# Kernel tuning notes

Hardware: AMD Instinct MI355X
Metric: run time of the kernel (lower is better)

## Reference

```python
import jax, jax.numpy as jnp
import numpy as np

EPS = 1e-5

def bn(x, p, axis):
    # p: (4,C) = [gamma, beta, running_mean, running_var]; eval-mode batchnorm
    g, b, m, v = p
    shp = [1] * x.ndim
    shp[axis] = -1
    g = g.reshape(shp); b = b.reshape(shp); m = m.reshape(shp); v = v.reshape(shp)
    return (x - m) * g * jax.lax.rsqrt(v + EPS) + b

def knn_idx(query, ref, k):
    # query (B,S,D), ref (B,N,D) -> (B,S,k) nearest-neighbor indices
    d = (jnp.sum(query * query, -1)[:, :, None]
         - 2.0 * jnp.einsum('bsd,bnd->bsn', query, ref)
         + jnp.sum(ref * ref, -1)[:, None, :])
    return jax.lax.top_k(-d, k)[1]

def fps(xyz, npoint):
    # farthest point sampling, deterministic start at index 0. xyz (B,N,3) -> (B,npoint)
    B, N, _ = xyz.shape
    def body(i, state):
        idxs, dists, far = state
        idxs = idxs.at[:, i].set(far)
        centroid = jnp.take_along_axis(xyz, far[:, None, None], axis=1)  # (B,1,3)
        d = jnp.sum((xyz - centroid) ** 2, -1)                           # (B,N)
        dists = jnp.minimum(dists, d)
        return idxs, dists, jnp.argmax(dists, -1).astype(jnp.int32)
    idxs = jnp.zeros((B, npoint), jnp.int32)
    dists = jnp.full((B, N), 1e10, xyz.dtype)
    far = jnp.zeros((B,), jnp.int32)
    idxs, _, _ = jax.lax.fori_loop(0, npoint, body, (idxs, dists, far))
    return idxs

def sample_and_group(npoint, nsample, xyz, feature):
    # xyz (B,N,3); feature (B,C,N) channel-first -> new_xyz (B,S,3), new_feature (B,S,k,2C)
    B = xyz.shape[0]
    xyz_sg = jax.lax.stop_gradient(xyz)
    fps_idx = fps(xyz_sg, npoint)                       # (B,S)
    bi = jnp.arange(B)[:, None]
    new_xyz = xyz[bi, fps_idx]                          # (B,S,3)
    ft = jnp.swapaxes(feature, 1, 2)                    # (B,N,C)
    new_pts = ft[bi, fps_idx]                           # (B,S,C)
    idx = knn_idx(jax.lax.stop_gradient(new_xyz), xyz_sg, nsample)  # (B,S,k)
    grouped = ft[jnp.arange(B)[:, None, None], idx]     # (B,S,k,C)
    centered = grouped - new_pts[:, :, None, :]
    new_feature = jnp.concatenate(
        [centered, jnp.broadcast_to(new_pts[:, :, None, :], grouped.shape)], -1)
    return new_xyz, new_feature

def local_op(x, w, bnp):
    # x (B,S,k,D); conv1d k=1 over D, bn, relu, max over neighbors -> (B,out,S)
    h = jax.nn.relu(bn(jnp.einsum('bskd,od->bsko', x, w), bnp, -1))
    return jnp.swapaxes(jnp.max(h, axis=2), 1, 2)

def edge_branch(f_t, idx, w, bnp):
    # DGCNN-style EdgeConv: concat(f_j - f_i, f_i), conv2d k=1, bn, leakyrelu, max over k
    B = f_t.shape[0]
    nb = f_t[jnp.arange(B)[:, None, None], idx]         # (B,N,k,C)
    center = jnp.broadcast_to(f_t[:, :, None, :], nb.shape)
    e = jnp.concatenate([nb - center, center], -1)      # (B,N,k,2C)
    h = jax.nn.leaky_relu(bn(jnp.einsum('bnkc,oc->bnko', e, w), bnp, -1), 0.2)
    return jnp.max(h, axis=2)                           # (B,N,C)

def dual_graph_fusion(xyz_cf, f, k, geo_w, geo_bn, feat_w, feat_bn, fuse_w, fuse_bn):
    # xyz_cf (B,3,N), f (B,C,N): one kNN graph in coordinate space, one in feature space,
    # EdgeConv on each, concat, 1x1 conv fusion -> (B,C,N)
    xyz_t = jax.lax.stop_gradient(jnp.swapaxes(xyz_cf, 1, 2))  # (B,N,3)
    f_t = jnp.swapaxes(f, 1, 2)                                # (B,N,C)
    idx_g = knn_idx(xyz_t, xyz_t, k)
    f_sg = jax.lax.stop_gradient(f_t)
    idx_f = knn_idx(f_sg, f_sg, k)
    g = edge_branch(f_t, idx_g, geo_w, geo_bn)
    h = edge_branch(f_t, idx_f, feat_w, feat_bn)
    fused = jnp.concatenate([g, h], -1)                        # (B,N,2C)
    out = jax.nn.leaky_relu(bn(jnp.einsum('bnc,oc->bno', fused, fuse_w), fuse_bn, -1), 0.2)
    return jnp.swapaxes(out, 1, 2)                             # (B,C,N)

def _bn_params(key, c):
    k1, k2, k3, k4 = jax.random.split(key, 4)
    g = jax.random.uniform(k1, (c,), minval=0.5, maxval=1.5)
    b = jax.random.normal(k2, (c,)) * 0.1
    m = jax.random.normal(k3, (c,)) * 0.1
    v = jax.random.uniform(k4, (c,), minval=0.5, maxval=1.5)
    return jnp.stack([g, b, m, v])

def setup_inputs() -> dict:
    key = jax.random.key(0)
    ks = jax.random.split(key, 20)
    B, N = 16, 2048
    def w(k, o, i):
        return jax.random.normal(k, (o, i), dtype=jnp.float32) * (1.0 / np.sqrt(i))
    return {
        'x': jax.random.normal(ks[0], (B, 6, N), dtype=jnp.float32),
        'w1': w(ks[1], 64, 6),        'bn1': _bn_params(ks[2], 64),
        'w2': w(ks[3], 1024, 64),     'bn2': _bn_params(ks[4], 1024),
        'geo_w': w(ks[5], 64, 128),   'geo_bn': _bn_params(ks[6], 64),
        'feat_w': w(ks[7], 64, 128),  'feat_bn': _bn_params(ks[8], 64),
        'fuse_w': w(ks[9], 64, 128),  'fuse_bn': _bn_params(ks[10], 64),
        'gl0_w': w(ks[11], 128, 128), 'gl0_bn': _bn_params(ks[12], 128),
        'gl1_w': w(ks[13], 256, 256), 'gl1_bn': _bn_params(ks[14], 256),
        'wf': w(ks[15], 512, 1280),   'bnf': _bn_params(ks[16], 512),
    }

def reference(x, w1, bn1, w2, bn2, geo_w, geo_bn, feat_w, feat_bn, fuse_w, fuse_bn,
              gl0_w, gl0_bn, gl1_w, gl1_bn, wf, bnf):
    B, _, N = x.shape
    xyz = jnp.swapaxes(x[:, 0:3, :], 1, 2)                                   # (B,N,3)
    f_o = jax.nn.relu(bn(jnp.einsum('bcn,oc->bon', x, w1), bn1, 1))          # (B,64,N)
    out_feat = dual_graph_fusion(x[:, 0:3, :], f_o, 20,
                                 geo_w, geo_bn, feat_w, feat_bn, fuse_w, fuse_bn)
    stride = N // 256
    x_skip = jax.nn.relu(bn(jnp.einsum('bcn,oc->bon', f_o[:, :, ::stride], w2), bn2, 1))  # (B,1024,256)
    new_xyz, nf = sample_and_group(512, 32, xyz, out_feat)
    f0 = local_op(nf, gl0_w, gl0_bn)                                         # (B,128,512)
    new_xyz, nf = sample_and_group(256, 32, new_xyz, f0)
    f1 = local_op(nf, gl1_w, gl1_bn)                                         # (B,256,256)
    f1 = jnp.concatenate([f1, x_skip], 1)                                    # (B,1280,256)
    res = jax.nn.leaky_relu(bn(jnp.einsum('bcn,oc->bon', f1, wf), bnf, 1), 0.2)  # (B,512,256)
    return res
```

## Files before the change

kernel.cpp:

```cpp
#include <hip/hip_runtime.h>
#include <float.h>
#include <math.h>


static constexpr int B_   = 16;
static constexpr int N_   = 2048;
static constexpr int NP1  = 512;
static constexpr int NP2  = 256;
static constexpr int KG   = 20;
static constexpr int NSAMP= 32;
static constexpr int CHQ  = 256;

static constexpr long OFF_FT   = 0;
static constexpr long OFF_SQ   = OFF_FT   + (long)B_*N_*64;
static constexpr long OFF_BIG  = OFF_SQ   + (long)B_*N_;
static constexpr long OFF_IDXG = OFF_BIG  + (long)B_*N_*256;
static constexpr long OFF_IDXF = OFF_IDXG + (long)B_*N_*KG;
static constexpr long OFF_OUTF = OFF_IDXF + (long)B_*N_*KG;
static constexpr long OFF_FPS1 = OFF_OUTF + (long)B_*N_*64;
static constexpr long OFF_NX1  = OFF_FPS1 + (long)B_*NP1;
static constexpr long OFF_IDX1 = OFF_NX1  + (long)B_*NP1*3;
static constexpr long OFF_F0T  = OFF_IDX1 + (long)B_*NP1*NSAMP;
static constexpr long OFF_FPS2 = OFF_F0T  + (long)B_*NP1*128;
static constexpr long OFF_NX2  = OFF_FPS2 + (long)B_*NP2;
static constexpr long OFF_IDX2 = OFF_NX2  + (long)B_*NP2*3;
static constexpr long OFF_Q1   = OFF_IDX2 + (long)B_*NP2*NSAMP;
static constexpr long OFF_V    = OFF_Q1   + (long)B_*NP1*512;
static constexpr long OFF_WPP  = OFF_V    + (long)B_*NP2*1280;
static constexpr long OFF_WPQ0 = OFF_WPP  + 256*64;
static constexpr long OFF_WPQ1 = OFF_WPQ0 + 256*64;
static constexpr long OFF_WFT  = OFF_WPQ1 + 512*128;
static constexpr long OFF_SC   = OFF_WFT  + 128*64;
static constexpr long OFF_DL1  = OFF_SC   + 4352;
static constexpr long OFF_DL2  = OFF_DL1  + (long)B_*256*8;
static constexpr long OFF_ST   = OFF_DL2  + (long)B_*512;
static constexpr long OFF_GSQ  = OFF_ST   + 256;

static constexpr int SC_S1=0, SC_T1=64, SC_SGEO=128, SC_TGEO=192, SC_SFEAT=256, SC_TFEAT=320,
   SC_SFUSE=384, SC_TFUSE=448, SC_SGL0=512, SC_TGL0=640, SC_SGL1=768, SC_TGL1=1024,
   SC_S2=1280, SC_T2=2304, SC_SF=3328, SC_TF=3840;

__device__ __forceinline__ float lrelu_(float x) { return x >= 0.0f ? x : 0.2f * x; }

template<int CTRL, int RM>
__device__ __forceinline__ float dpp_maxm(float v) {
    int o = __builtin_amdgcn_update_dpp(__float_as_int(v), __float_as_int(v),
                                        CTRL, RM, 0xF, false);
    return fmaxf(v, __int_as_float(o));
}
__device__ __forceinline__ float wave_max64_sgpr(float v) {
    v = dpp_maxm<0xB1, 0xF>(v);
    v = dpp_maxm<0x4E, 0xF>(v);
    v = dpp_maxm<0x141,0xF>(v);
    v = dpp_maxm<0x140,0xF>(v);
    v = dpp_maxm<0x142,0xA>(v);
    v = dpp_maxm<0x143,0xC>(v);
    return __int_as_float(__builtin_amdgcn_readlane(__float_as_int(v), 63));
}

template<int CTRL>
__device__ __forceinline__ unsigned dpp_minu(unsigned x) {
    unsigned o = (unsigned)__builtin_amdgcn_update_dpp(0, (int)x, CTRL, 0xF, 0xF, true);
    return o < x ? o : x;
}
__device__ __forceinline__ unsigned wave_minu(unsigned x) {
    x = dpp_minu<0xB1>(x);
    x = dpp_minu<0x4E>(x);
    x = dpp_minu<0x141>(x);
    x = dpp_minu<0x140>(x);
    { unsigned o = (unsigned)__shfl_xor((int)x, 16); x = o < x ? o : x; }
    { unsigned o = (unsigned)__shfl_xor((int)x, 32); x = o < x ? o : x; }
    return x;
}

__device__ __forceinline__ unsigned sortable_(float f) {
    unsigned u = __float_as_uint(f);
    return u ^ ((unsigned)((int)u >> 31) | 0x80000000u);
}

__global__ void k_prep(const float* __restrict__ bn1, const float* __restrict__ bn2,
                       const float* __restrict__ geow, const float* __restrict__ geobn,
                       const float* __restrict__ featw, const float* __restrict__ featbn,
                       const float* __restrict__ fusew, const float* __restrict__ fusebn,
                       const float* __restrict__ gl0w, const float* __restrict__ gl0bn,
                       const float* __restrict__ gl1w, const float* __restrict__ gl1bn,
                       const float* __restrict__ bnfp, float* __restrict__ ws)
{
    const int tid = blockIdx.x * blockDim.x + threadIdx.x;
    const int nt  = gridDim.x * blockDim.x;
    float* sc = ws + OFF_SC;
    {
        const float* ps[8]  = {bn1, geobn, featbn, fusebn, gl0bn, gl1bn, bn2, bnfp};
        const int    ch[8]  = {64, 64, 64, 64, 128, 256, 1024, 512};
        const int    so[8]  = {SC_S1, SC_SGEO, SC_SFEAT, SC_SFUSE, SC_SGL0, SC_SGL1, SC_S2, SC_SF};
        const int    to[8]  = {SC_T1, SC_TGEO, SC_TFEAT, SC_TFUSE, SC_TGL0, SC_TGL1, SC_T2, SC_TF};
        for (int g = 0; g < 8; g++) {
            const float* p = ps[g]; int C = ch[g];
            for (int i = tid; i < C; i += nt) {
                float gg = p[i], bb = p[C+i], mm = p[2*C+i], vv = p[3*C+i];
                float s = gg * (1.0f / sqrtf(vv + 1e-5f));
                sc[so[g] + i] = s;
                sc[to[g] + i] = bb - mm * s;
            }
        }
    }
    for (int j = tid; j < 256*64; j += nt) {
        int o = j >> 6, c = j & 63; float v;
        if      (o < 64)  v = geow[o*128 + c];
        else if (o < 128) v = geow[(o-64)*128 + 64 + c];
        else if (o < 192) v = featw[(o-128)*128 + c];
        else              v = featw[(o-192)*128 + 64 + c];
        ws[OFF_WPP + j] = v;
    }
    for (int j = tid; j < 256*64; j += nt) {
        int o = j >> 6, c = j & 63; float v;
        if (o < 128) v = gl0w[o*128 + c];
        else         v = gl0w[(o-128)*128 + 64 + c] - gl0w[(o-128)*128 + c];
        ws[OFF_WPQ0 + j] = v;
    }
    for (int j = tid; j < 512*128; j += nt) {
        int o = j >> 7, c = j & 127; float v;
        if (o < 256) v = gl1w[o*256 + c];
        else         v = gl1w[(o-256)*256 + 128 + c] - gl1w[(o-256)*256 + c];
        ws[OFF_WPQ1 + j] = v;
    }
    for (int j = tid; j < 128*64; j += nt) {
        int c = j >> 6, o = j & 63;
        ws[OFF_WFT + j] = fusew[o*128 + c];
    }
}

__global__ void __launch_bounds__(256) k_feat0(const float* __restrict__ x,
                                               const float* __restrict__ w1,
                                               const float* __restrict__ sc,
                                               float* __restrict__ ft, float* __restrict__ sq,
                                               float* __restrict__ gsq)
{
    const int t = threadIdx.x, lane = t & 63, w = t >> 6;
    const int pid = blockIdx.x*4 + w;
    const int b = pid >> 11, n = pid & (N_-1);
    const float* xb = x + (long)b*6*N_ + n;
    float acc = 0.0f;
    #pragma unroll
    for (int c = 0; c < 6; c++) acc += w1[lane*6 + c] * xb[(long)c*N_];
    float val = fmaxf(sc[SC_S1 + lane]*acc + sc[SC_T1 + lane], 0.0f);
    ft[((long)b*N_ + n)*64 + lane] = val;
    float v2 = val*val;
    #pragma unroll
    for (int s = 1; s < 64; s <<= 1) v2 += __shfl_xor(v2, s);
    if (lane == 0) {
        sq[b*N_ + n] = v2;
        float rx = xb[0], ry = xb[N_], rz = xb[2*N_];
        gsq[b*N_ + n] = __fadd_rn(__fadd_rn(__fmul_rn(rx,rx), __fmul_rn(ry,ry)),
                                  __fmul_rn(rz,rz));
    }
}

template<int RPL, int KSEL>
__device__ __forceinline__ void topk_sel3(float (&v)[RPL], int lane, int* __restrict__ out)
{
    unsigned key[RPL];
    #pragma unroll
    for (int j = 0; j < RPL; j++) key[j] = sortable_(v[j]);

    unsigned consumed = 0;
    unsigned m1 = key[0]; int s1 = 0;
    unsigned m2 = 0xFFFFFFFFu; int s2 = 0;
    #pragma unroll
    for (int j = 1; j < RPL; j++) {
        unsigned kk = key[j];
        bool lt1 = kk < m1;
        bool lt2 = kk < m2;
        unsigned nm2 = lt1 ? m1 : (lt2 ? kk : m2);
        int      ns2 = lt1 ? s1 : (lt2 ? j  : s2);
        m1 = lt1 ? kk : m1;
        s1 = lt1 ? j  : s1;
        m2 = nm2; s2 = ns2;
    }
    #pragma unroll 1
    for (int k = 0; k < KSEL; k++) {
        unsigned g = wave_minu(m1);
        unsigned long long cand = __ballot(m1 == g);
        int gi;
        if (__popcll(cand) > 1) {
            int ci = (m1 == g) ? (s1*64 + lane) : 0x7FFFFFFF;
            #pragma unroll
            for (int s = 1; s < 64; s <<= 1) { int o = __shfl_xor(ci, s); ci = o < ci ? o : ci; }
            gi = ci;
        } else {
            int wl = __ffsll((long long)cand) - 1;
            gi = __builtin_amdgcn_readlane(s1, wl) * 64 + wl;
        }
        if (lane == 0) out[k] = gi;
        if (k + 1 < KSEL) {
            bool win = (m1 == g) && (s1*64 + lane == gi);
            if (win) {
                consumed |= 1u << s1;
                m1 = m2; s1 = s2;
                m2 = 0xFFFFFFFFu;
            }
            bool need = win && (m1 == 0xFFFFFFFFu);
            if (__any(need)) {
                if (need) {
                    m1 = 0xFFFFFFFFu; s1 = 0; m2 = 0xFFFFFFFFu; s2 = 0;
                    #pragma unroll
                    for (int j = 0; j < RPL; j++) {
                        unsigned kk = ((consumed >> j) & 1u) ? 0xFFFFFFFFu : key[j];
                        bool lt1 = kk < m1;
                        bool lt2 = kk < m2;
                        unsigned nm2 = lt1 ? m1 : (lt2 ? kk : m2);
                        int      ns2 = lt1 ? s1 : (lt2 ? j  : s2);
                        m1 = lt1 ? kk : m1;
                        s1 = lt1 ? j  : s1;
                        m2 = nm2; s2 = ns2;
                    }
                }
            }
        }
    }
}

template<int NREF, int RPL, int KSEL, bool RSQ>
__device__ __forceinline__ void knn_gbody(
    const float* qp, long qBatch, int qsN, int qsD, int NQ,
    const float* rp, long rBatch, long rsN, long rsD,
    const float* rsq, long rsqBatch,
    int* out, int bid)
{
    const int t = threadIdx.x, lane = t & 63, w = t >> 6;
    const int bpb = NQ / 4;
    const int b = bid / bpb;
    const int qi = (bid % bpb)*4 + w;
    const float* rb = rp + (long)b*rBatch;
    const float* qb = qp + (long)b*qBatch + (long)qi*qsN;
    float qx = qb[0], qy = qb[qsD], qz = qb[2*qsD];
    float sumq = __fadd_rn(__fadd_rn(__fmul_rn(qx,qx), __fmul_rn(qy,qy)), __fmul_rn(qz,qz));
    float v[RPL];
    #pragma unroll
    for (int j = 0; j < RPL; j++) {
        long n = j*64 + lane;
        float rx = rb[n*rsN];
        float ry = rb[n*rsN + rsD];
        float rz = rb[n*rsN + 2*rsD];
        float dot = __fadd_rn(__fadd_rn(__fmul_rn(qx,rx), __fmul_rn(qy,ry)), __fmul_rn(qz,rz));
        float sumr;
        if constexpr (RSQ) sumr = rsq[(long)b*rsqBatch + n];
        else sumr = __fadd_rn(__fadd_rn(__fmul_rn(rx,rx), __fmul_rn(ry,ry)), __fmul_rn(rz,rz));
        v[j] = __fadd_rn(__fsub_rn(sumq, __fmul_rn(2.0f, dot)), sumr);
    }
    topk_sel3<RPL, KSEL>(v, lane, out + ((long)b*NQ + qi)*KSEL);
}

__device__ __forceinline__ void fps1_seg_body(
    const float* __restrict__ x, int b, int i0, int cnt,
    int* __restrict__ fps1, float* __restrict__ nx1,
    float* __restrict__ dl1s, float* __restrict__ st, float* __restrict__ smem)
{
    __builtin_amdgcn_s_setprio(3);
    const int t = threadIdx.x, lane = t & 63, wave = t >> 6;
    const float* pb = x + (long)b*6*N_;

    float4* mrgc   = (float4*)smem;
    int*    mrgi   = (int*)(smem + 32);
    int*    sidxsg = (int*)(smem + 40);
    float*  mxsg   = smem + 296;
    float*  mysg   = smem + 552;
    float*  mzsg   = smem + 808;

    float px[8], py[8], pz[8], dl[8];
    {
        const float4* a4  = (const float4*)(pb + 8*t);
        const float4* b4  = (const float4*)(pb + N_ + 8*t);
        const float4* c4p = (const float4*)(pb + 2*N_ + 8*t);
        float4 a0 = a4[0], a1 = a4[1];
        float4 b0 = b4[0], b1 = b4[1];
        float4 c0 = c4p[0], c1 = c4p[1];
        px[0]=a0.x; px[1]=a0.y; px[2]=a0.z; px[3]=a0.w;
        px[4]=a1.x; px[5]=a1.y; px[6]=a1.z; px[7]=a1.w;
        py[0]=b0.x; py[1]=b0.y; py[2]=b0.z; py[3]=b0.w;
        py[4]=b1.x; py[5]=b1.y; py[6]=b1.z; py[7]=b1.w;
        pz[0]=c0.x; pz[1]=c0.y; pz[2]=c0.z; pz[3]=c0.w;
        pz[4]=c1.x; pz[5]=c1.y; pz[6]=c1.z; pz[7]=c1.w;
    }
    int far; float cx, cy, cz;
    if (i0 == 0) {
        #pragma unroll
        for (int p = 0; p < 8; p++) dl[p] = 1e10f;
        far = 0; cx = pb[0]; cy = pb[N_]; cz = pb[2*N_];
    } else {
        const float4* ds = (const float4*)(dl1s + ((long)b*256 + t)*8);
        float4 d0 = ds[0], d1 = ds[1];
        dl[0]=d0.x; dl[1]=d0.y; dl[2]=d0.z; dl[3]=d0.w;
        dl[4]=d1.x; dl[5]=d1.y; dl[6]=d1.z; dl[7]=d1.w;
        far = __float_as_int(st[b*16+0]);
        cx = st[b*16+1]; cy = st[b*16+2]; cz = st[b*16+3];
    }

    for (int k = 0; k < cnt; k++) {
        if (t == 0) { sidxsg[k] = far; mxsg[k] = cx; mysg[k] = cy; mzsg[k] = cz; }
        float bv = -1.0f; int bp = 0;
        #pragma unroll
        for (int p = 0; p < 8; p++) {
            float dx = __fsub_rn(px[p], cx);
            float dy = __fsub_rn(py[p], cy);
            float dz = __fsub_rn(pz[p], cz);
            float d  = __fadd_rn(__fadd_rn(__fmul_rn(dx,dx), __fmul_rn(dy,dy)), __fmul_rn(dz,dz));
            float nd = fminf(dl[p], d);
            dl[p] = nd;
            if (nd > bv) { bv = nd; bp = p; }
        }
        float wx = px[0], wy = py[0], wz = pz[0];
        #pragma unroll
        for (int p = 1; p < 8; p++) {
            bool c = (bp == p);
            wx = c ? px[p] : wx; wy = c ? py[p] : wy; wz = c ? pz[p] : wz;
        }
        float gm = wave_max64_sgpr(bv);
        unsigned long long cand = __ballot(bv == gm);
        int wl = __ffsll((long long)cand) - 1;
        int   wbp = __builtin_amdgcn_readlane(bp, wl);
        float sxw = __int_as_float(__builtin_amdgcn_readlane(__float_as_int(wx), wl));
        float syw = __int_as_float(__builtin_amdgcn_readlane(__float_as_int(wy), wl));
        float szw = __int_as_float(__builtin_amdgcn_readlane(__float_as_int(wz), wl));
        int par = k & 1;
        if (lane == 0) {
            mrgc[par*4 + wave] = make_float4(sxw, syw, szw, gm);
            mrgi[par*4 + wave] = (((wave << 6) | wl) << 3) + wbp;
        }
        __syncthreads();
        float4 e0 = mrgc[par*4 + 0];
        float fv = e0.w; int fi = mrgi[par*4 + 0];
        float ncx = e0.x, ncy = e0.y, ncz = e0.z;
        #pragma unroll
// ... 153 lines not shown
        acc[1][0] += a.y*b4.x; acc[1][1] += a.y*b4.y; acc[1][2] += a.y*b4.z; acc[1][3] += a.y*b4.w;
        acc[2][0] += a.z*b4.x; acc[2][1] += a.z*b4.y; acc[2][2] += a.z*b4.z; acc[2][3] += a.z*b4.w;
        acc[3][0] += a.w*b4.x; acc[3][1] += a.w*b4.y; acc[3][2] += a.w*b4.z; acc[3][3] += a.w*b4.w;
    }
    const int i0 = ib*64 + ty*4;
    const int j0 = jb*64 + tx*4;
    #pragma unroll
    for (int ii = 0; ii < 4; ii++) {
        float sqq = sqb[qbNew + i0 + ii];
        #pragma unroll
        for (int jj = 0; jj < 4; jj++) {
            int r = j0 + jj;
            Dnew[((long)b*CHQ + i0 + ii)*N_ + r] = (sqq - 2.0f*acc[ii][jj]) + sqb[r];
        }
    }
}

__device__ __forceinline__ void proj64_body(
    int gi, int nIB, int nJB,
    const float* __restrict__ A, long aBatch, int aRow,
    const float* __restrict__ Bw,
    float* __restrict__ C, long cBatch, int cRow, int cCol0,
    int act, const float* __restrict__ sv, const float* __restrict__ tv,
    float* __restrict__ smem)
{
    float* As = smem;
    float* Bs = smem + 4096;
    const int ib = gi % nIB;
    const int jb = (gi / nIB) % nJB;
    const int b  = gi / (nIB*nJB);
    const int t  = threadIdx.x;
    const int tx = t & 15, ty = t >> 4;
    const float* Ab = A + (long)b*aBatch + (long)(ib*64)*aRow;
    #pragma unroll
    for (int m = 0; m < 4; m++) {
        int li = t + m*256; int r = li >> 4; int c4 = li & 15;
        int cs = r ^ ((c4 & 7) << 2);
        float4 av = *(const float4*)(Ab + (long)r*aRow + c4*4);
        As[(c4*4+0)*64 + cs] = av.x; As[(c4*4+1)*64 + cs] = av.y;
        As[(c4*4+2)*64 + cs] = av.z; As[(c4*4+3)*64 + cs] = av.w;
        float4 bv = *(const float4*)(Bw + (long)(jb*64 + r)*64 + c4*4);
        Bs[(c4*4+0)*64 + cs] = bv.x; Bs[(c4*4+1)*64 + cs] = bv.y;
        Bs[(c4*4+2)*64 + cs] = bv.z; Bs[(c4*4+3)*64 + cs] = bv.w;
    }
    __syncthreads();
    float acc[4][4];
    #pragma unroll
    for (int i = 0; i < 4; i++)
        #pragma unroll
        for (int j = 0; j < 4; j++) acc[i][j] = 0.0f;
    #pragma unroll 4
    for (int k = 0; k < 64; k++) {
        int s4 = ((k >> 2) & 7) << 2;
        float4 a  = *(const float4*)&As[k*64 + ((ty*4) ^ s4)];
        float4 b4 = *(const float4*)&Bs[k*64 + ((tx*4) ^ s4)];
        acc[0][0] += a.x*b4.x; acc[0][1] += a.x*b4.y; acc[0][2] += a.x*b4.z; acc[0][3] += a.x*b4.w;
        acc[1][0] += a.y*b4.x; acc[1][1] += a.y*b4.y; acc[1][2] += a.y*b4.z; acc[1][3] += a.y*b4.w;
        acc[2][0] += a.z*b4.x; acc[2][1] += a.z*b4.y; acc[2][2] += a.z*b4.z; acc[2][3] += a.z*b4.w;
        acc[3][0] += a.w*b4.x; acc[3][1] += a.w*b4.y; acc[3][2] += a.w*b4.z; acc[3][3] += a.w*b4.w;
    }
    const int i0 = ib*64 + ty*4;
    const int j0 = jb*64 + tx*4;
    #pragma unroll
    for (int ii = 0; ii < 4; ii++)
        #pragma unroll
        for (int jj = 0; jj < 4; jj++) {
            int j = j0 + jj;
            float vv = acc[ii][jj];
            if (act == 1) vv = fmaxf(sv[j]*vv + tv[j], 0.0f);
            C[(long)b*cBatch + (long)(i0+ii)*cRow + cCol0 + j] = vv;
        }
}

__device__ __forceinline__ void sel_body(
    const float* __restrict__ Dold, int qbOld, int* __restrict__ idxf, int bid)
{
    const int t = threadIdx.x, lane = t & 63, w = t >> 6;
    const int r = bid*4 + w;
    const int b = r >> 8, qi = r & (CHQ-1);
    const float* row = Dold + ((long)b*CHQ + qi) * N_;
    float v[32];
    #pragma unroll
    for (int j = 0; j < 32; j++) v[j] = row[j*64 + lane];
    topk_sel3<32, KG>(v, lane, idxf + ((long)b*N_ + qbOld + qi)*KG);
}

__device__ __forceinline__ void edgefuse_body(
    const float* __restrict__ P, const int* __restrict__ idxg, const int* __restrict__ idxf,
    const float* __restrict__ wft, const float* __restrict__ sc,
    float* __restrict__ outf, int bid, float* __restrict__ smem)
{
    float* wt = smem;
    float* fused = smem + 8192;
    const int t = threadIdx.x, lane = t & 63, w = t >> 6;
    for (int i = t; i < 128*64; i += 256) wt[i] = wft[i];
    const int pid = bid*4 + w;
    const int b = pid >> 11, n = pid & (N_-1);
    const float* Prow = P + ((long)b*N_ + n)*256;
    const int* ig  = idxg + ((long)b*N_ + n)*KG;
    const int* ifx = idxf + ((long)b*N_ + n)*KG;
    float gmax = -FLT_MAX, hmax = -FLT_MAX;
    for (int k = 0; k < KG; k++) {
        int idg = ig[k];
        gmax = fmaxf(gmax, P[((long)b*N_ + idg)*256 + lane]);
        int idf = ifx[k];
        hmax = fmaxf(hmax, P[((long)b*N_ + idf)*256 + 128 + lane]);
    }
    float glin = gmax - Prow[lane]       + Prow[64 + lane];
    float hlin = hmax - Prow[128 + lane] + Prow[192 + lane];
    float gv = lrelu_(sc[SC_SGEO + lane]*glin + sc[SC_TGEO + lane]);
    float hv = lrelu_(sc[SC_SFEAT + lane]*hlin + sc[SC_TFEAT + lane]);
    fused[w*128 + lane]      = gv;
    fused[w*128 + 64 + lane] = hv;
    __syncthreads();
    float acc = 0.0f;
    #pragma unroll 8
    for (int c4 = 0; c4 < 32; c4++) {
        float4 f = *(const float4*)&fused[w*128 + c4*4];
        acc += f.x * wt[(c4*4+0)*64 + lane];
        acc += f.y * wt[(c4*4+1)*64 + lane];
        acc += f.z * wt[(c4*4+2)*64 + lane];
        acc += f.w * wt[(c4*4+3)*64 + lane];
    }
    float ov = lrelu_(sc[SC_SFUSE + lane]*acc + sc[SC_TFUSE + lane]);
    outf[((long)b*N_ + n)*64 + lane] = ov;
}

template<int QN, int ROWW, int CO, int MROWS, int SO>
__device__ __forceinline__ void gathermax_body(
    const float* __restrict__ Q, const int* __restrict__ knn, const int* __restrict__ fpsi,
    const float* __restrict__ sv, const float* __restrict__ tv,
    float* __restrict__ outp, int outRow, int bid)
{
    const int t = threadIdx.x, lane = t & 63, w = t >> 6;
    const int pid = bid*4 + w;
    const int b = pid / SO, s = pid % SO;
    const int* ix = knn + ((long)b*SO + s)*NSAMP;
    float mx[QN];
    #pragma unroll
    for (int q = 0; q < QN; q++) mx[q] = -FLT_MAX;
    for (int k = 0; k < NSAMP; k++) {
        int id = ix[k];
        const float* r = Q + ((long)b*MROWS + id)*ROWW;
        #pragma unroll
        for (int q = 0; q < QN; q++) mx[q] = fmaxf(mx[q], r[lane + 64*q]);
    }
    int crow = fpsi[b*SO + s];
    const float* cr = Q + ((long)b*MROWS + crow)*ROWW + CO;
    #pragma unroll
    for (int q = 0; q < QN; q++) {
        int o = lane + 64*q;
        float lin = mx[q] + cr[o];
        float val = fmaxf(sv[o]*lin + tv[o], 0.0f);
        outp[((long)b*SO + s)*outRow + o] = val;
    }
}

__global__ void __launch_bounds__(256, 4) k_geo0(
    const float* __restrict__ x, int* __restrict__ idxg,
    int* __restrict__ fps1, float* __restrict__ nx1,
    float* __restrict__ dl1s, float* __restrict__ st,
    const float* __restrict__ ft, const float* __restrict__ sq,
    const float* __restrict__ gsq, float* __restrict__ D0)
{
    __shared__ float smem[8192];
    if (blockIdx.x < (unsigned)B_) {
        fps1_seg_body(x, blockIdx.x, 0, 256, fps1, nx1, dl1s, st, smem);
        return;
    }
    if (blockIdx.x < (unsigned)(B_ + 8192)) {
        knn_gbody<N_,32,KG,true>(x, (long)6*N_, 1, N_, N_,
                                 x, (long)6*N_, 1, N_,
                                 gsq, (long)N_, idxg, blockIdx.x - B_);
        return;
    }
    dist_gemm_body(ft, sq, D0, 0, blockIdx.x - (B_ + 8192), smem);
}

__global__ void __launch_bounds__(256, 4) k_chain(
    const float* __restrict__ x, const float* __restrict__ ft, const float* __restrict__ sq,
    float* __restrict__ Dnew, int qbNew,
    const float* __restrict__ Dold, int qbOld,
    int* __restrict__ idxf,
    int* __restrict__ fps1, float* __restrict__ nx1,
    float* __restrict__ dl1s, float* __restrict__ st, int i0)
{
    __shared__ float smem[8192];
    if (blockIdx.x < 16u) {
        fps1_seg_body(x, blockIdx.x, i0, 32, fps1, nx1, dl1s, st, smem);
        return;
    }
    if (blockIdx.x < 1040u) {
        sel_body(Dold, qbOld, idxf, blockIdx.x - 16);
        return;
    }
    dist_gemm_body(ft, sq, Dnew, qbNew, blockIdx.x - 1040, smem);
}

__global__ void __launch_bounds__(256, 4) k_tail9(
    const float* __restrict__ x, const float* __restrict__ ft,
    const float* __restrict__ Dold, int qbOld, int* __restrict__ idxf,
    int* __restrict__ fps1, float* __restrict__ nx1,
    float* __restrict__ dl1s, float* __restrict__ st,
    const float* __restrict__ wpp, float* __restrict__ big)
{
    __shared__ float smem[8192];
    if (blockIdx.x < 16u) {
        fps1_seg_body(x, blockIdx.x, 480, 32, fps1, nx1, dl1s, st, smem);
        return;
    }
    if (blockIdx.x < 1040u) {
        sel_body(Dold, qbOld, idxf, blockIdx.x - 16);
        return;
    }
    proj64_body(blockIdx.x - 1040, 32, 4, ft, (long)N_*64, 64, wpp,
                big, (long)N_*256, 256, 0, 0, nullptr, nullptr, smem);
}

__global__ void __launch_bounds__(256, 4) k_tail10(
    const float* __restrict__ nx1, int* __restrict__ fps2, float* __restrict__ nx2,
    float* __restrict__ dl2s, float* __restrict__ st,
    const float* __restrict__ P, const int* __restrict__ idxg, const int* __restrict__ idxf,
    const float* __restrict__ wft, const float* __restrict__ sc, float* __restrict__ outf,
    const float* __restrict__ ft, const float* __restrict__ w2, float* __restrict__ V)
{
    __shared__ float smem[8704];
    if (blockIdx.x < 16u) {
        fps2_seg_body(blockIdx.x, 0, 128, nx1, fps2, nx2, dl2s, st, smem);
        return;
    }
    if (blockIdx.x < (unsigned)(16 + 8192)) {
        edgefuse_body(P, idxg, idxf, wft, sc, outf, blockIdx.x - 16, smem);
        return;
    }
    proj64_body(blockIdx.x - (16 + 8192), 4, 16, ft, (long)N_*64, 512, w2,
                V, (long)NP2*1280, 1280, 256, 1, sc + SC_S2, sc + SC_T2, smem);
}

__global__ void __launch_bounds__(256, 4) k_tail11(
    const float* __restrict__ nx1, int* __restrict__ fps2, float* __restrict__ nx2,
    float* __restrict__ dl2s, float* __restrict__ st,
    const float* __restrict__ x, const float* __restrict__ gsq, int* __restrict__ idx1,
    const float* __restrict__ outf, const float* __restrict__ wpq0, float* __restrict__ big)
{
    __shared__ float smem[8192];
    if (blockIdx.x < 16u) {
        fps2_seg_body(blockIdx.x, 128, 128, nx1, fps2, nx2, dl2s, st, smem);
        return;
    }
    if (blockIdx.x < (unsigned)(16 + 2048)) {
        knn_gbody<2048,32,32,true>(nx1, (long)NP1*3, 3, 1, NP1,
                                   x, (long)6*N_, (long)1, (long)N_,
                                   gsq, (long)N_, idx1, blockIdx.x - 16);
        return;
    }
    proj64_body(blockIdx.x - (16 + 2048), 32, 4, outf, (long)N_*64, 64, wpq0,
                big, (long)N_*256, 256, 0, 0, nullptr, nullptr, smem);
}

__global__ void __launch_bounds__(256, 4) k_gm0knn2(
    const float* __restrict__ big, const int* __restrict__ idx1, const int* __restrict__ fps1,
    const float* __restrict__ sc, float* __restrict__ f0t,
    const float* __restrict__ nx2, const float* __restrict__ nx1, int* __restrict__ idx2)
{
    if (blockIdx.x < 2048u) {
        gathermax_body<2,256,128,2048,512>(big, idx1, fps1,
            sc + SC_SGL0, sc + SC_TGL0, f0t, 128, blockIdx.x);
        return;
    }
    knn_gbody<512,8,32,false>(nx2, (long)NP2*3, 3, 1, NP2,
                              nx1, (long)NP1*3, (long)3, (long)1,
                              nullptr, 0, idx2, blockIdx.x - 2048);
}

__global__ void __launch_bounds__(256) k_gemm(
    const float* __restrict__ A, long aBatch, int aRow,
    const float* __restrict__ Bw, long bBatch, int K,
    float* __restrict__ C, long cBatch, int cRow, int cCol0,
    int act, const float* __restrict__ sv, const float* __restrict__ tv,
    int epi)
{
    __shared__ float As[4096];
    __shared__ float Bs[4096];
    const int b  = blockIdx.z;
    const int ib = blockIdx.x * 64;
    const int jb = blockIdx.y * 64;
    const int t  = threadIdx.x;
    const int tx = t & 15, ty = t >> 4;
    const float* Ab = A + (long)b * aBatch;
    const float* Bb = Bw + (long)b * bBatch;
    float acc[4][4];
    #pragma unroll
    for (int i = 0; i < 4; i++)
        #pragma unroll
        for (int j = 0; j < 4; j++) acc[i][j] = 0.0f;

    for (int kb = 0; kb < K; kb += 64) {
        #pragma unroll
        for (int m = 0; m < 4; m++) {
            int li = t + m*256; int r = li >> 4; int c4 = li & 15;
            int cs = r ^ ((c4 & 7) << 2);
            float4 av = *(const float4*)(Ab + (long)(ib + r)*aRow + kb + c4*4);
            As[(c4*4+0)*64 + cs] = av.x; As[(c4*4+1)*64 + cs] = av.y;
            As[(c4*4+2)*64 + cs] = av.z; As[(c4*4+3)*64 + cs] = av.w;
            float4 bv = *(const float4*)(Bb + (long)(jb + r)*K + kb + c4*4);
            Bs[(c4*4+0)*64 + cs] = bv.x; Bs[(c4*4+1)*64 + cs] = bv.y;
            Bs[(c4*4+2)*64 + cs] = bv.z; Bs[(c4*4+3)*64 + cs] = bv.w;
        }
        __syncthreads();
        #pragma unroll 4
        for (int k = 0; k < 64; k++) {
            int s4 = ((k >> 2) & 7) << 2;
            float4 a  = *(const float4*)&As[k*64 + ((ty*4) ^ s4)];
            float4 b4 = *(const float4*)&Bs[k*64 + ((tx*4) ^ s4)];
            acc[0][0] += a.x*b4.x; acc[0][1] += a.x*b4.y; acc[0][2] += a.x*b4.z; acc[0][3] += a.x*b4.w;
            acc[1][0] += a.y*b4.x; acc[1][1] += a.y*b4.y; acc[1][2] += a.y*b4.z; acc[1][3] += a.y*b4.w;
            acc[2][0] += a.z*b4.x; acc[2][1] += a.z*b4.y; acc[2][2] += a.z*b4.z; acc[2][3] += a.z*b4.w;
            acc[3][0] += a.w*b4.x; acc[3][1] += a.w*b4.y; acc[3][2] += a.w*b4.z; acc[3][3] += a.w*b4.w;
        }
        __syncthreads();
    }

    const int i0 = ib + ty*4;
    const int j0 = jb + tx*4;
    if (epi == 2) {
        #pragma unroll
        for (int ii = 0; ii < 4; ii++)
            #pragma unroll
            for (int jj = 0; jj < 4; jj++) {
                int j = j0 + jj;
                float vv = lrelu_(sv[j]*acc[ii][jj] + tv[j]);
                C[(long)b*cBatch + (long)j*cRow + (i0+ii)] = vv;
            }
    } else {
        #pragma unroll
        for (int ii = 0; ii < 4; ii++)
            #pragma unroll
            for (int jj = 0; jj < 4; jj++) {
                int j = j0 + jj;
                float vv = acc[ii][jj];
                if (act == 1) vv = fmaxf(sv[j]*vv + tv[j], 0.0f);
                else if (act == 2) vv = lrelu_(sv[j]*vv + tv[j]);
                C[(long)b*cBatch + (long)(i0+ii)*cRow + cCol0 + j] = vv;
            }
    }
}

template<int QN, int ROWW, int CO, int MROWS, int SO>
__global__ void __launch_bounds__(256) k_gathermax(
    const float* __restrict__ Q, const int* __restrict__ knn, const int* __restrict__ fpsi,
    const float* __restrict__ sv, const float* __restrict__ tv,
    float* __restrict__ outp, int outRow)
{
    gathermax_body<QN,ROWW,CO,MROWS,SO>(Q, knn, fpsi, sv, tv, outp, outRow, blockIdx.x);
}

extern "C" void kernel_launch(void* const* d_in, const int* in_sizes, int n_in,
                              void* d_out, int out_size, void* d_ws, size_t ws_size,
                              hipStream_t stream)
{
    const float* x      = (const float*)d_in[0];
    const float* w1     = (const float*)d_in[1];
    const float* bn1    = (const float*)d_in[2];
    const float* w2     = (const float*)d_in[3];
    const float* bn2    = (const float*)d_in[4];
    const float* geow   = (const float*)d_in[5];
    const float* geobn  = (const float*)d_in[6];
    const float* featw  = (const float*)d_in[7];
    const float* featbn = (const float*)d_in[8];
    const float* fusew  = (const float*)d_in[9];
    const float* fusebn = (const float*)d_in[10];
    const float* gl0w   = (const float*)d_in[11];
    const float* gl0bn  = (const float*)d_in[12];
    const float* gl1w   = (const float*)d_in[13];
    const float* gl1bn  = (const float*)d_in[14];
    const float* wf     = (const float*)d_in[15];
    const float* bnfp   = (const float*)d_in[16];

    float* ws  = (float*)d_ws;
    float* out = (float*)d_out;

    float* FT   = ws + OFF_FT;
    float* SQ   = ws + OFF_SQ;
    float* BIG  = ws + OFF_BIG;
    int*   IDXG = (int*)(ws + OFF_IDXG);
    int*   IDXF = (int*)(ws + OFF_IDXF);
    float* OUTF = ws + OFF_OUTF;
    int*   FPS1 = (int*)(ws + OFF_FPS1);
    float* NX1  = ws + OFF_NX1;
    int*   IDX1 = (int*)(ws + OFF_IDX1);
    float* F0T  = ws + OFF_F0T;
    int*   FPS2 = (int*)(ws + OFF_FPS2);
    float* NX2  = ws + OFF_NX2;
    int*   IDX2 = (int*)(ws + OFF_IDX2);
    float* Q1B  = ws + OFF_Q1;
    float* V    = ws + OFF_V;
    float* WPP  = ws + OFF_WPP;
    float* WPQ0 = ws + OFF_WPQ0;
    float* WPQ1 = ws + OFF_WPQ1;
    float* WFT  = ws + OFF_WFT;
    float* SC   = ws + OFF_SC;
    float* DL1  = ws + OFF_DL1;
    float* DL2  = ws + OFF_DL2;
    float* ST   = ws + OFF_ST;
    float* GSQ  = ws + OFF_GSQ;

    hipLaunchKernelGGL(k_prep, dim3(64), dim3(256), 0, stream,
        bn1, bn2, geow, geobn, featw, featbn, fusew, fusebn, gl0w, gl0bn, gl1w, gl1bn, bnfp, ws);

    hipLaunchKernelGGL(k_feat0, dim3(B_*N_/4), dim3(256), 0, stream, x, w1, SC, FT, SQ, GSQ);

    hipLaunchKernelGGL(k_geo0, dim3(B_ + 8192 + 2048), dim3(256), 0, stream,
        x, IDXG, FPS1, NX1, DL1, ST, FT, SQ, GSQ, BIG);

    float* bufs[2] = { BIG, Q1B };
    for (int ci = 1; ci < 8; ci++) {
        hipLaunchKernelGGL(k_chain, dim3(16 + 1024 + 2048), dim3(256), 0, stream,
            x, FT, SQ,
            bufs[ci & 1], ci*CHQ,
            bufs[(ci - 1) & 1], (ci - 1)*CHQ,
            IDXF, FPS1, NX1, DL1, ST, 256 + 32*(ci - 1));
    }

    hipLaunchKernelGGL(k_tail9, dim3(16 + 1024 + 2048), dim3(256), 0, stream,
        x, FT, bufs[1], 7*CHQ, IDXF, FPS1, NX1, DL1, ST, WPP, BIG);

    hipLaunchKernelGGL(k_tail10, dim3(16 + 8192 + 1024), dim3(256), 0, stream,
        NX1, FPS2, NX2, DL2, ST,
        BIG, IDXG, IDXF, WFT, SC, OUTF,
        FT, w2, V);

    hipLaunchKernelGGL(k_tail11, dim3(16 + 2048 + 2048), dim3(256), 0, stream,
        NX1, FPS2, NX2, DL2, ST,
        x, GSQ, IDX1,
        OUTF, WPQ0, BIG);

    hipLaunchKernelGGL(k_gm0knn2, dim3(2048 + 1024), dim3(256), 0, stream,
        BIG, IDX1, FPS1, SC, F0T, NX2, NX1, IDX2);

    hipLaunchKernelGGL(k_gemm, dim3(NP1/64, 512/64, B_), dim3(256), 0, stream,
        F0T, (long)NP1*128, 128, WPQ1, (long)0, 128,
        Q1B, (long)NP1*512, 512, 0, 0, nullptr, nullptr, 0);

    hipLaunchKernelGGL((k_gathermax<4,512,256,512,256>), dim3(B_*NP2/4), dim3(256), 0, stream,
        Q1B, IDX2, FPS2, SC + SC_SGL1, SC + SC_TGL1, V, 1280);

    hipLaunchKernelGGL(k_gemm, dim3(NP2/64, 512/64, B_), dim3(256), 0, stream,
        V, (long)NP2*1280, 1280, wf, (long)0, 1280,
        out, (long)512*256, 256, 0, 2, SC + SC_SF, SC + SC_TF, 2);

    (void)in_sizes; (void)n_in; (void)out_size; (void)ws_size;
}
```

Measured before the change: 660.5 us.

## Pack xyz into float4, fuse prep/feat0 launch, deepen top-k candidate cache

Merges the prep and first-feature kernels into one launch. Point coordinates are now stored with their squared norm as a packed float4, so the kNN kernels do one vector load per reference point instead of four strided loads. The top-k selector now keeps three candidates per lane instead of two, which makes full rescans rarer. It also reduces the wave minimum with DPP row broadcasts and a readlane, and gathers results in registers for a single coalesced store. The cost is extra registers per lane and a little more work per compare step.

```diff
diff --git a/kernel.cpp b/kernel.cpp
--- a/kernel.cpp
+++ b/kernel.cpp
@@ -34,7 +34,7 @@
 static constexpr long OFF_DL1  = OFF_SC   + 4352;
 static constexpr long OFF_DL2  = OFF_DL1  + (long)B_*256*8;
 static constexpr long OFF_ST   = OFF_DL2  + (long)B_*512;
-static constexpr long OFF_GSQ  = OFF_ST   + 256;
+static constexpr long OFF_XYZ4 = OFF_ST   + 256;
 
 static constexpr int SC_S1=0, SC_T1=64, SC_SGEO=128, SC_TGEO=192, SC_SFEAT=256, SC_TFEAT=320,
    SC_SFUSE=384, SC_TFUSE=448, SC_SGL0=512, SC_TGL0=640, SC_SGL1=768, SC_TGL1=1024,
@@ -58,19 +58,19 @@
     return __int_as_float(__builtin_amdgcn_readlane(__float_as_int(v), 63));
 }
 
-template<int CTRL>
-__device__ __forceinline__ unsigned dpp_minu(unsigned x) {
-    unsigned o = (unsigned)__builtin_amdgcn_update_dpp(0, (int)x, CTRL, 0xF, 0xF, true);
+template<int CTRL, int RM>
+__device__ __forceinline__ unsigned dpp_minm(unsigned x) {
+    unsigned o = (unsigned)__builtin_amdgcn_update_dpp((int)x, (int)x, CTRL, RM, 0xF, false);
     return o < x ? o : x;
 }
-__device__ __forceinline__ unsigned wave_minu(unsigned x) {
-    x = dpp_minu<0xB1>(x);
-    x = dpp_minu<0x4E>(x);
-    x = dpp_minu<0x141>(x);
-    x = dpp_minu<0x140>(x);
-    { unsigned o = (unsigned)__shfl_xor((int)x, 16); x = o < x ? o : x; }
-    { unsigned o = (unsigned)__shfl_xor((int)x, 32); x = o < x ? o : x; }
-    return x;
+__device__ __forceinline__ unsigned wave_minu_sgpr(unsigned x) {
+    x = dpp_minm<0xB1, 0xF>(x);
+    x = dpp_minm<0x4E, 0xF>(x);
+    x = dpp_minm<0x141,0xF>(x);
+    x = dpp_minm<0x140,0xF>(x);
+    x = dpp_minm<0x142,0xA>(x);
+    x = dpp_minm<0x143,0xC>(x);
+    return (unsigned)__builtin_amdgcn_readlane((int)x, 63);
 }
 
 __device__ __forceinline__ unsigned sortable_(float f) {
@@ -78,16 +78,17 @@
     return u ^ ((unsigned)((int)u >> 31) | 0x80000000u);
 }
 
-__global__ void k_prep(const float* __restrict__ bn1, const float* __restrict__ bn2,
-                       const float* __restrict__ geow, const float* __restrict__ geobn,
-                       const float* __restrict__ featw, const float* __restrict__ featbn,
-                       const float* __restrict__ fusew, const float* __restrict__ fusebn,
-                       const float* __restrict__ gl0w, const float* __restrict__ gl0bn,
-                       const float* __restrict__ gl1w, const float* __restrict__ gl1bn,
-                       const float* __restrict__ bnfp, float* __restrict__ ws)
-{
-    const int tid = blockIdx.x * blockDim.x + threadIdx.x;
-    const int nt  = gridDim.x * blockDim.x;
+__device__ __forceinline__ void prep_body(
+    const float* bn1, const float* bn2,
+    const float* geow, const float* geobn,
+    const float* featw, const float* featbn,
+    const float* fusew, const float* fusebn,
+    const float* gl0w, const float* gl0bn,
+    const float* gl1w, const float* gl1bn,
+    const float* bnfp, float* ws, int bid)
+{
+    const int tid = bid * 256 + threadIdx.x;
+    const int nt  = 64 * 256;
     float* sc = ws + OFF_SC;
     {
         const float* ps[8]  = {bn1, geobn, featbn, fusebn, gl0bn, gl1bn, bn2, bnfp};
@@ -130,56 +131,81 @@
     }
 }
 
-__global__ void __launch_bounds__(256) k_feat0(const float* __restrict__ x,
-                                               const float* __restrict__ w1,
-                                               const float* __restrict__ sc,
-                                               float* __restrict__ ft, float* __restrict__ sq,
-                                               float* __restrict__ gsq)
+__device__ __forceinline__ void feat0_body(
+    const float* __restrict__ x, const float* __restrict__ w1,
+    const float* __restrict__ bn1,
+    float* __restrict__ ft, float* __restrict__ sq,
+    float4* __restrict__ xyz4, int bid)
 {
     const int t = threadIdx.x, lane = t & 63, w = t >> 6;
-    const int pid = blockIdx.x*4 + w;
+    const int pid = bid*4 + w;
     const int b = pid >> 11, n = pid & (N_-1);
     const float* xb = x + (long)b*6*N_ + n;
     float acc = 0.0f;
     #pragma unroll
     for (int c = 0; c < 6; c++) acc += w1[lane*6 + c] * xb[(long)c*N_];
-    float val = fmaxf(sc[SC_S1 + lane]*acc + sc[SC_T1 + lane], 0.0f);
+    float gg = bn1[lane], bb = bn1[64+lane], mm = bn1[128+lane], vv = bn1[192+lane];
+    float s = gg * (1.0f / sqrtf(vv + 1e-5f));
+    float tt = bb - mm * s;
+    float val = fmaxf(s*acc + tt, 0.0f);
     ft[((long)b*N_ + n)*64 + lane] = val;
     float v2 = val*val;
     #pragma unroll
-    for (int s = 1; s < 64; s <<= 1) v2 += __shfl_xor(v2, s);
+    for (int sft = 1; sft < 64; sft <<= 1) v2 += __shfl_xor(v2, sft);
     if (lane == 0) {
         sq[b*N_ + n] = v2;
         float rx = xb[0], ry = xb[N_], rz = xb[2*N_];
-        gsq[b*N_ + n] = __fadd_rn(__fadd_rn(__fmul_rn(rx,rx), __fmul_rn(ry,ry)),
-                                  __fmul_rn(rz,rz));
-    }
+        float g2 = __fadd_rn(__fadd_rn(__fmul_rn(rx,rx), __fmul_rn(ry,ry)), __fmul_rn(rz,rz));
+        xyz4[(long)b*N_ + n] = make_float4(rx, ry, rz, g2);
+    }
+}
+
+__global__ void __launch_bounds__(256) k_init(
+    const float* __restrict__ x, const float* __restrict__ w1,
+    const float* bn1, const float* bn2,
+    const float* geow, const float* geobn,
+    const float* featw, const float* featbn,
+    const float* fusew, const float* fusebn,
+    const float* gl0w, const float* gl0bn,
+    const float* gl1w, const float* gl1bn,
+    const float* bnfp, float* ws,
+    float* __restrict__ ft, float* __restrict__ sq, float4* __restrict__ xyz4)
+{
+    if (blockIdx.x < 64u) {
+        prep_body(bn1, bn2, geow, geobn, featw, featbn, fusew, fusebn,
+                  gl0w, gl0bn, gl1w, gl1bn, bnfp, ws, blockIdx.x);
+        return;
+    }
+    feat0_body(x, w1, bn1, ft, sq, xyz4, blockIdx.x - 64);
 }
 
 template<int RPL, int KSEL>
-__device__ __forceinline__ void topk_sel3(float (&v)[RPL], int lane, int* __restrict__ out)
+__device__ __forceinline__ void topk_sel4(float (&v)[RPL], int lane, int* __restrict__ out)
 {
     unsigned key[RPL];
     #pragma unroll
     for (int j = 0; j < RPL; j++) key[j] = sortable_(v[j]);
 
     unsigned consumed = 0;
-    unsigned m1 = key[0]; int s1 = 0;
-    unsigned m2 = 0xFFFFFFFFu; int s2 = 0;
-    #pragma unroll
-    for (int j = 1; j < RPL; j++) {
+    unsigned m1 = 0xFFFFFFFFu, m2 = 0xFFFFFFFFu, m3 = 0xFFFFFFFFu;
+    int s1 = 0, s2 = 0, s3 = 0;
+    #pragma unroll
+    for (int j = 0; j < RPL; j++) {
         unsigned kk = key[j];
-        bool lt1 = kk < m1;
-        bool lt2 = kk < m2;
+        bool lt1 = kk < m1, lt2 = kk < m2, lt3 = kk < m3;
+        unsigned nm3 = lt2 ? m2 : (lt3 ? kk : m3);
+        int      ns3 = lt2 ? s2 : (lt3 ? j  : s3);
         unsigned nm2 = lt1 ? m1 : (lt2 ? kk : m2);
         int      ns2 = lt1 ? s1 : (lt2 ? j  : s2);
         m1 = lt1 ? kk : m1;
         s1 = lt1 ? j  : s1;
-        m2 = nm2; s2 = ns2;
-    }
+        m2 = nm2; s2 = ns2; m3 = nm3; s3 = ns3;
+    }
+
+    int keep = 0;
     #pragma unroll 1
     for (int k = 0; k < KSEL; k++) {
-        unsigned g = wave_minu(m1);
+        unsigned g = wave_minu_sgpr(m1);
         unsigned long long cand = __ballot(m1 == g);
         int gi;
         if (__popcll(cand) > 1) {
@@ -191,40 +217,73 @@
             int wl = __ffsll((long long)cand) - 1;
             gi = __builtin_amdgcn_readlane(s1, wl) * 64 + wl;
         }
-        if (lane == 0) out[k] = gi;
+        keep = (lane == k) ? gi : keep;
         if (k + 1 < KSEL) {
             bool win = (m1 == g) && (s1*64 + lane == gi);
             if (win) {
                 consumed |= 1u << s1;
                 m1 = m2; s1 = s2;
-                m2 = 0xFFFFFFFFu;
+                m2 = m3; s2 = s3;
+                m3 = 0xFFFFFFFFu;
             }
             bool need = win && (m1 == 0xFFFFFFFFu);
             if (__any(need)) {
                 if (need) {
-                    m1 = 0xFFFFFFFFu; s1 = 0; m2 = 0xFFFFFFFFu; s2 = 0;
+                    m1 = 0xFFFFFFFFu; m2 = 0xFFFFFFFFu; m3 = 0xFFFFFFFFu;
+                    s1 = 0; s2 = 0; s3 = 0;
                     #pragma unroll
                     for (int j = 0; j < RPL; j++) {
                         unsigned kk = ((consumed >> j) & 1u) ? 0xFFFFFFFFu : key[j];
-                        bool lt1 = kk < m1;
-                        bool lt2 = kk < m2;
+                        bool lt1 = kk < m1, lt2 = kk < m2, lt3 = kk < m3;
+                        unsigned nm3 = lt2 ? m2 : (lt3 ? kk : m3);
+                        int      ns3 = lt2 ? s2 : (lt3 ? j  : s3);
                         unsigned nm2 = lt1 ? m1 : (lt2 ? kk : m2);
                         int      ns2 = lt1 ? s1 : (lt2 ? j  : s2);
                         m1 = lt1 ? kk : m1;
                         s1 = lt1 ? j  : s1;
-                        m2 = nm2; s2 = ns2;
+                        m2 = nm2; s2 = ns2; m3 = nm3; s3 = ns3;
                     }
                 }
             }
         }
     }
-}
-
-template<int NREF, int RPL, int KSEL, bool RSQ>
+    if (lane < KSEL) out[lane] = keep;
+}
+
+template<int RPL, int KSEL, bool QX4>
+__device__ __forceinline__ void knn_x4body(
+    const float4* __restrict__ xyz4, int NQ,
+    const float* __restrict__ qp, long qBatch, int qsN,
+    int* __restrict__ out, int bid)
+{
+    const int t = threadIdx.x, lane = t & 63, w = t >> 6;
+    const int bpb = NQ / 4;
+    const int b = bid / bpb;
+    const int qi = (bid % bpb)*4 + w;
+    const float4* rb = xyz4 + (long)b*N_;
+    float qx, qy, qz, sumq;
+    if constexpr (QX4) {
+        float4 q = rb[qi];
+        qx = q.x; qy = q.y; qz = q.z; sumq = q.w;
+    } else {
+        const float* qb = qp + (long)b*qBatch + (long)qi*qsN;
+        qx = qb[0]; qy = qb[1]; qz = qb[2];
+        sumq = __fadd_rn(__fadd_rn(__fmul_rn(qx,qx), __fmul_rn(qy,qy)), __fmul_rn(qz,qz));
+    }
+    float v[RPL];
+    #pragma unroll
+    for (int j = 0; j < RPL; j++) {
+        float4 r = rb[j*64 + lane];
+        float dot = __fadd_rn(__fadd_rn(__fmul_rn(qx,r.x), __fmul_rn(qy,r.y)), __fmul_rn(qz,r.z));
+        v[j] = __fadd_rn(__fsub_rn(sumq, __fmul_rn(2.0f, dot)), r.w);
+    }
+    topk_sel4<RPL, KSEL>(v, lane, out + ((long)b*NQ + qi)*KSEL);
+}
+
+template<int RPL, int KSEL>
 __device__ __forceinline__ void knn_gbody(
-    const float* qp, long qBatch, int qsN, int qsD, int NQ,
-    const float* rp, long rBatch, long rsN, long rsD,
-    const float* rsq, long rsqBatch,
+    const float* qp, long qBatch, int qsN, int NQ,
+    const float* rp, long rBatch, int rsN,
     int* out, int bid)
 {
     const int t = threadIdx.x, lane = t & 63, w = t >> 6;
@@ -233,22 +292,18 @@
     const int qi = (bid % bpb)*4 + w;
     const float* rb = rp + (long)b*rBatch;
     const float* qb = qp + (long)b*qBatch + (long)qi*qsN;
-    float qx = qb[0], qy = qb[qsD], qz = qb[2*qsD];
+    float qx = qb[0], qy = qb[1], qz = qb[2];
     float sumq = __fadd_rn(__fadd_rn(__fmul_rn(qx,qx), __fmul_rn(qy,qy)), __fmul_rn(qz,qz));
     float v[RPL];
     #pragma unroll
     for (int j = 0; j < RPL; j++) {
         long n = j*64 + lane;
-        float rx = rb[n*rsN];
-        float ry = rb[n*rsN + rsD];
-        float rz = rb[n*rsN + 2*rsD];
+        float rx = rb[n*rsN], ry = rb[n*rsN + 1], rz = rb[n*rsN + 2];
         float dot = __fadd_rn(__fadd_rn(__fmul_rn(qx,rx), __fmul_rn(qy,ry)), __fmul_rn(qz,rz));
-        float sumr;
-        if constexpr (RSQ) sumr = rsq[(long)b*rsqBatch + n];
-        else sumr = __fadd_rn(__fadd_rn(__fmul_rn(rx,rx), __fmul_rn(ry,ry)), __fmul_rn(rz,rz));
+        float sumr = __fadd_rn(__fadd_rn(__fmul_rn(rx,rx), __fmul_rn(ry,ry)), __fmul_rn(rz,rz));
         v[j] = __fadd_rn(__fsub_rn(sumq, __fmul_rn(2.0f, dot)), sumr);
     }
-    topk_sel3<RPL, KSEL>(v, lane, out + ((long)b*NQ + qi)*KSEL);
+    topk_sel4<RPL, KSEL>(v, lane, out + ((long)b*NQ + qi)*KSEL);
 }
 
 __device__ __forceinline__ void fps1_seg_body(
@@ -568,7 +623,7 @@
     float v[32];
     #pragma unroll
     for (int j = 0; j < 32; j++) v[j] = row[j*64 + lane];
-    topk_sel3<32, KG>(v, lane, idxf + ((long)b*N_ + qbOld + qi)*KG);
+    topk_sel4<32, KG>(v, lane, idxf + ((long)b*N_ + qbOld + qi)*KG);
 }
 
 __device__ __forceinline__ void edgefuse_body(
@@ -643,11 +698,12 @@
 }
 
 __global__ void __launch_bounds__(256, 4) k_geo0(
-    const float* __restrict__ x, int* __restrict__ idxg,
+    const float* __restrict__ x, const float4* __restrict__ xyz4,
+    int* __restrict__ idxg,
     int* __restrict__ fps1, float* __restrict__ nx1,
     float* __restrict__ dl1s, float* __restrict__ st,
     const float* __restrict__ ft, const float* __restrict__ sq,
-    const float* __restrict__ gsq, float* __restrict__ D0)
+    float* __restrict__ D0)
 {
     __shared__ float smem[8192];
     if (blockIdx.x < (unsigned)B_) {
@@ -655,9 +711,7 @@
         return;
     }
     if (blockIdx.x < (unsigned)(B_ + 8192)) {
-        knn_gbody<N_,32,KG,true>(x, (long)6*N_, 1, N_, N_,
-                                 x, (long)6*N_, 1, N_,
-                                 gsq, (long)N_, idxg, blockIdx.x - B_);
+        knn_x4body<32, KG, true>(xyz4, N_, nullptr, 0, 0, idxg, blockIdx.x - B_);
         return;
     }
     dist_gemm_body(ft, sq, D0, 0, blockIdx.x - (B_ + 8192), smem);
@@ -726,7 +780,7 @@
 __global__ void __launch_bounds__(256, 4) k_tail11(
     const float* __restrict__ nx1, int* __restrict__ fps2, float* __restrict__ nx2,
     float* __restrict__ dl2s, float* __restrict__ st,
-    const float* __restrict__ x, const float* __restrict__ gsq, int* __restrict__ idx1,
+    const float4* __restrict__ xyz4, int* __restrict__ idx1,
     const float* __restrict__ outf, const float* __restrict__ wpq0, float* __restrict__ big)
 {
     __shared__ float smem[8192];
@@ -735,9 +789,7 @@
         return;
     }
     if (blockIdx.x < (unsigned)(16 + 2048)) {
-        knn_gbody<2048,32,32,true>(nx1, (long)NP1*3, 3, 1, NP1,
-                                   x, (long)6*N_, (long)1, (long)N_,
-                                   gsq, (long)N_, idx1, blockIdx.x - 16);
+        knn_x4body<32, 32, false>(xyz4, NP1, nx1, (long)NP1*3, 3, idx1, blockIdx.x - 16);
         return;
     }
     proj64_body(blockIdx.x - (16 + 2048), 32, 4, outf, (long)N_*64, 64, wpq0,
@@ -754,9 +806,8 @@
             sc + SC_SGL0, sc + SC_TGL0, f0t, 128, blockIdx.x);
         return;
     }
-    knn_gbody<512,8,32,false>(nx2, (long)NP2*3, 3, 1, NP2,
-                              nx1, (long)NP1*3, (long)3, (long)1,
-                              nullptr, 0, idx2, blockIdx.x - 2048);
+    knn_gbody<8,32>(nx2, (long)NP2*3, 3, NP2,
+                    nx1, (long)NP1*3, 3, idx2, blockIdx.x - 2048);
 }
 
 __global__ void __launch_bounds__(256) k_gemm(
@@ -889,15 +940,14 @@
     float* DL1  = ws + OFF_DL1;
     float* DL2  = ws + OFF_DL2;
     float* ST   = ws + OFF_ST;
-    float* GSQ  = ws + OFF_GSQ;
-
-    hipLaunchKernelGGL(k_prep, dim3(64), dim3(256), 0, stream,
-        bn1, bn2, geow, geobn, featw, featbn, fusew, fusebn, gl0w, gl0bn, gl1w, gl1bn, bnfp, ws);
-
-    hipLaunchKernelGGL(k_feat0, dim3(B_*N_/4), dim3(256), 0, stream, x, w1, SC, FT, SQ, GSQ);
+    float4* XYZ4 = (float4*)(ws + OFF_XYZ4);
+
+    hipLaunchKernelGGL(k_init, dim3(64 + B_*N_/4), dim3(256), 0, stream,
+        x, w1, bn1, bn2, geow, geobn, featw, featbn, fusew, fusebn,
+        gl0w, gl0bn, gl1w, gl1bn, bnfp, ws, FT, SQ, XYZ4);
 
     hipLaunchKernelGGL(k_geo0, dim3(B_ + 8192 + 2048), dim3(256), 0, stream,
-        x, IDXG, FPS1, NX1, DL1, ST, FT, SQ, GSQ, BIG);
+        x, XYZ4, IDXG, FPS1, NX1, DL1, ST, FT, SQ, BIG);
 
     float* bufs[2] = { BIG, Q1B };
     for (int ci = 1; ci < 8; ci++) {
@@ -918,7 +968,7 @@
 
     hipLaunchKernelGGL(k_tail11, dim3(16 + 2048 + 2048), dim3(256), 0, stream,
         NX1, FPS2, NX2, DL2, ST,
-        x, GSQ, IDX1,
+        XYZ4, IDX1,
         OUTF, WPQ0, BIG);
 
     hipLaunchKernelGGL(k_gm0knn2, dim3(2048 + 1024), dim3(256), 0, stream,
```

Result: faster. 621.5 us (-5.9%).
